# Kernel tuning notes

Measured on AMD Instinct MI355X. Metric: run time of the kernel, lower is better.

The kernel has to match this reference:

```python
import jax, jax.numpy as jnp
import numpy as np

B, SORB, H, L = 32768, 64, 256, 2


def setup_inputs() -> dict:
    key = jax.random.key(0)
    ks = jax.random.split(key, 11)
    s = 1.0 / np.sqrt(H)

    def u(k, shape):
        return jax.random.uniform(k, shape, jnp.float32, -s, s)

    return {
        "x": jax.random.randint(ks[0], (B, SORB), 0, 2).astype(jnp.int32),
        # PyTorch GRU params, gate order (r, z, n); layer 0 input_size=2, layer 1 input_size=H
        "w_ih0": u(ks[1], (3 * H, 2)), "w_hh0": u(ks[2], (3 * H, H)),
        "b_ih0": u(ks[3], (3 * H,)), "b_hh0": u(ks[4], (3 * H,)),
        "w_ih1": u(ks[5], (3 * H, H)), "w_hh1": u(ks[6], (3 * H, H)),
        "b_ih1": u(ks[7], (3 * H,)), "b_hh1": u(ks[8], (3 * H,)),
        "w_amp": u(ks[9], (2, H)), "b_amp": u(ks[10], (2,)),
    }


def _gru_cell(x, h, w_ih, w_hh, b_ih, b_hh):
    # PyTorch GRUCell math, gates in (r, z, n) order
    gi = x @ w_ih.T + b_ih
    gh = h @ w_hh.T + b_hh
    ir, iz, i_n = jnp.split(gi, 3, axis=-1)
    hr, hz, h_n = jnp.split(gh, 3, axis=-1)
    r = jax.nn.sigmoid(ir + hr)
    z = jax.nn.sigmoid(iz + hz)
    n = jnp.tanh(i_n + r * h_n)
    return (1.0 - z) * n + z * h


def reference(x, w_ih0, w_hh0, b_ih0, b_hh0, w_ih1, w_hh1, b_ih1, b_hh1, w_amp, b_amp):
    bits = x  # [B, SORB], values in {0,1} (equals ((+-1)+1)/2 of original input)
    nb = bits.shape[0]
    layer_params = [(w_ih0, w_hh0, b_ih0, b_hh0), (w_ih1, w_hh1, b_ih1, b_hh1)]

    def stacked(inp, h):  # h: [L, B, H]
        hs = []
        for l, (wi, wh, bi, bh) in enumerate(layer_params):
            hl = _gru_cell(inp, h[l], wi, wh, bi, bh)
            hs.append(hl)
            inp = hl
        return inp, jnp.stack(hs)

    h0 = jnp.zeros((L, nb, H), jnp.float32)
    # priming step with zero input (x0 = zeros(nbatch,1,2))
    _, h = stacked(jnp.zeros((nb, 2), jnp.float32), h0)

    def step(h, b_t):  # b_t: [B]
        onehot = jax.nn.one_hot(b_t, 2, dtype=jnp.float32)
        y, h = stacked(onehot, h)
        amp = jax.nn.softmax(y @ w_amp.T + b_amp, axis=1)  # [B, 2]
        p = jnp.sum(amp * onehot, axis=1)  # conditional prob of the sampled bit
        return h, p

    _, probs = jax.lax.scan(step, h, bits.T)  # probs: [SORB, B]
    return jnp.sqrt(jnp.prod(probs, axis=0))  # wavefunction amplitude, [B]
```

## Files before the change

kernel.cpp:

```cpp
#include <hip/hip_runtime.h>

typedef _Float16 f16;
typedef _Float16 f16x8 __attribute__((ext_vector_type(8)));
typedef float f32x4 __attribute__((ext_vector_type(4)));

#define H_    256
#define TB_   64
#define NT_   1024
#define SORB_ 64
#define SLOT_ 8192

#define MFMA16(a, b, c) __builtin_amdgcn_mfma_f32_16x16x32_f16((a), (b), (c), 0, 0, 0)
#define UNR _Pragma("unroll")

__device__ __forceinline__ float sigm(float v) {
  return __builtin_amdgcn_rcpf(1.0f + __builtin_amdgcn_exp2f(v * -1.442695040888963f));
}
__device__ __forceinline__ float tanh_fast(float v) {
  float a = fabsf(v);
  float e = __builtin_amdgcn_exp2f(a * -2.885390081777927f);
  float t = (1.0f - e) * __builtin_amdgcn_rcpf(1.0f + e);
  return copysignf(t, v);
}
__device__ __forceinline__ int lswz(int lrow, int col) {
  return lrow * H_ + (col ^ ((lrow & 7) << 3));
}

__global__ void wcvt(const float* __restrict__ a, const float* __restrict__ b,
                     const float* __restrict__ c, f16* __restrict__ o) {
  int i = blockIdx.x * 256 + threadIdx.x;
  const int n = 768 * 256;
  if (i < n) {
    o[i]         = (f16)a[i];
    o[n + i]     = (f16)b[i];
    o[2 * n + i] = (f16)c[i];
  }
}

__global__ __launch_bounds__(NT_, 4) void rnnwf(
    const int* __restrict__ x,
    const float* __restrict__ w_ih0, const float* __restrict__ b_ih0,
    const float* __restrict__ b_hh0, const float* __restrict__ b_ih1,
    const float* __restrict__ b_hh1, const float* __restrict__ w_amp,
    const float* __restrict__ b_amp, const f16* __restrict__ W16,
    float* __restrict__ out)
{
  __shared__ __align__(16) f16 hall[6 * SLOT_];
  __shared__ float wampL[512];
  __shared__ unsigned short bitsL[TB_ * 4];
  __shared__ unsigned long long bitsT[SORB_];

  const int tid  = threadIdx.x;
  const int wave = tid >> 6;
  const int lane = tid & 63;
  const int l15  = lane & 15;
  const int lg   = lane >> 4;
  const int lg4  = lg << 2;
  const int col  = wave * 16 + l15;
  const int rowbase = blockIdx.x * TB_;

  for (int j = tid; j < 512; j += NT_) wampL[j] = w_amp[j];
  if (tid < 256) {
    int row = tid >> 2, q = tid & 3;
    const int* xp = x + (size_t)(rowbase + row) * SORB_ + q * 16;
    unsigned m = 0;
    #pragma unroll
    for (int i = 0; i < 16; ++i) m |= (unsigned)(xp[i] & 1) << i;
    bitsL[row * 4 + q] = (unsigned short)m;
  }
  for (int i = tid; i < 6 * SLOT_; i += NT_) hall[i] = (f16)0.f;

  const float baseR = b_ih0[col]       + b_hh0[col];
  const float baseZ = b_ih0[256 + col] + b_hh0[256 + col];
  const float baseN = b_ih0[512 + col];
  const float wR0 = w_ih0[2 * col + 0],         wR1 = w_ih0[2 * col + 1];
  const float wZ0 = w_ih0[2 * (256 + col) + 0], wZ1 = w_ih0[2 * (256 + col) + 1];
  const float wN0 = w_ih0[2 * (512 + col) + 0], wN1 = w_ih0[2 * (512 + col) + 1];
  const float sumR0 = baseR + wR0, dR = wR1 - wR0;
  const float sumZ0 = baseZ + wZ0, dZ = wZ1 - wZ0;
  const float sumN0 = baseN + wN0, dN = wN1 - wN0;
  const float bhh0n_c = b_hh0[512 + col];
  const float b1r_c   = b_ih1[col]       + b_hh1[col];
  const float b1z_c   = b_ih1[256 + col] + b_hh1[256 + col];
  const float b1ni_c  = b_ih1[512 + col];
  const float b1nh_c  = b_hh1[512 + col];
  const float ba0 = b_amp[0], ba1 = b_amp[1];
  __syncthreads();

  if (tid < SORB_) {
    unsigned long long mk = 0ull;
    const int q = tid >> 4, sh = tid & 15;
    #pragma unroll 4
    for (int r = 0; r < TB_; ++r)
      mk |= (unsigned long long)((bitsL[r * 4 + q] >> sh) & 1) << r;
    bitsT[tid] = mk;
  }
  __syncthreads();

  float prob = 1.0f;
  const f16* Wih1 = W16 + 768 * 256;
  const f16* Whh1 = W16 + 2 * 768 * 256;
  const f16* p0base = W16  + col * 256;
  const f16* pibase = Wih1 + col * 256;
  const f16* phbase = Whh1 + col * 256;

  const int hrow = tid >> 4;
  const int t16  = tid & 15;
  const int hsh  = hrow & 31;
  const bool hhi = hrow >= 32;

  int pa = 0, pb = 2 * SLOT_, pc = 4 * SLOT_;

  for (int t = -1; t < SORB_; ++t) {
    unsigned lo32 = 0u, hi32 = 0u;
    if (t >= 0) {
      unsigned long long mk = bitsT[t];
      lo32 = (unsigned)mk; hi32 = (unsigned)(mk >> 32);
    }

    {
      f32x4 aR[4], aZ[4], aN[4];
      UNR for (int m = 0; m < 4; ++m) { aR[m] = (f32x4){0,0,0,0}; aZ[m] = aR[m]; aN[m] = aR[m]; }
      #pragma unroll 2
      for (int kt = 0; kt < 8; ++kt) {
        const int k0 = kt * 32 + lg * 8;
        f16x8 Br = *(const f16x8*)(p0base + k0);
        f16x8 Bz = *(const f16x8*)(p0base + 65536 + k0);
        f16x8 Bn = *(const f16x8*)(p0base + 131072 + k0);
        UNR for (int m = 0; m < 4; ++m) {
          f16x8 A = *(const f16x8*)&hall[pa + (m >> 1) * SLOT_ + lswz((m & 1) * 16 + l15, k0)];
          aR[m] = MFMA16(A, Br, aR[m]);
          aZ[m] = MFMA16(A, Bz, aZ[m]);
          aN[m] = MFMA16(A, Bn, aN[m]);
        }
      }
      if (t >= 0) {
        UNR for (int m = 0; m < 4; ++m) {
          const unsigned hsel = (m < 2) ? lo32 : hi32;
          UNR for (int e = 0; e < 4; ++e) {
            const int lrow = (m & 1) * 16 + lg4 + e;
            float fb = (float)((hsel >> ((m & 1) * 16 + lg4 + e)) & 1u);
            float giR = fmaf(fb, dR, sumR0);
            float giZ = fmaf(fb, dZ, sumZ0);
            float giN = fmaf(fb, dN, sumN0);
            float r  = sigm(aR[m][e] + giR);
            float z  = sigm(aZ[m][e] + giZ);
            float n  = tanh_fast(giN + r * (aN[m][e] + bhh0n_c));
            float ho = (float)hall[pa + (m >> 1) * SLOT_ + lswz(lrow, col)];
            hall[pc + (m >> 1) * SLOT_ + lswz(lrow, col)] = (f16)((1.0f - z) * n + z * ho);
          }
        }
      } else {
        UNR for (int m = 0; m < 4; ++m) {
          UNR for (int e = 0; e < 4; ++e) {
            const int lrow = (m & 1) * 16 + lg4 + e;
            float r  = sigm(aR[m][e] + baseR);
            float z  = sigm(aZ[m][e] + baseZ);
            float n  = tanh_fast(baseN + r * (aN[m][e] + bhh0n_c));
            float ho = (float)hall[pa + (m >> 1) * SLOT_ + lswz(lrow, col)];
            hall[pc + (m >> 1) * SLOT_ + lswz(lrow, col)] = (f16)((1.0f - z) * n + z * ho);
          }
        }
      }
    }
    __syncthreads();

    {
      f32x4 tR[4], tZ[4], tNi[4], tNh[4];
      UNR for (int m = 0; m < 4; ++m) {
        tR[m] = (f32x4){0,0,0,0}; tZ[m] = tR[m]; tNi[m] = tR[m]; tNh[m] = tR[m];
      }
      #pragma unroll 1
      for (int kt = 0; kt < 8; ++kt) {
        const int k0 = kt * 32 + lg * 8;
        {
          f16x8 BiR = *(const f16x8*)(pibase + k0);
          f16x8 BiZ = *(const f16x8*)(pibase + 65536 + k0);
          f16x8 BiN = *(const f16x8*)(pibase + 131072 + k0);
          UNR for (int m = 0; m < 4; ++m) {
            f16x8 A0 = *(const f16x8*)&hall[pc + (m >> 1) * SLOT_ + lswz((m & 1) * 16 + l15, k0)];
            tR[m]  = MFMA16(A0, BiR, tR[m]);
            tZ[m]  = MFMA16(A0, BiZ, tZ[m]);
            tNi[m] = MFMA16(A0, BiN, tNi[m]);
          }
        }
        {
          f16x8 BhR = *(const f16x8*)(phbase + k0);
          f16x8 BhZ = *(const f16x8*)(phbase + 65536 + k0);
          f16x8 BhN = *(const f16x8*)(phbase + 131072 + k0);
          UNR for (int m = 0; m < 4; ++m) {
            f16x8 A1 = *(const f16x8*)&hall[pb + (m >> 1) * SLOT_ + lswz((m & 1) * 16 + l15, k0)];
            tR[m]  = MFMA16(A1, BhR, tR[m]);
            tZ[m]  = MFMA16(A1, BhZ, tZ[m]);
            tNh[m] = MFMA16(A1, BhN, tNh[m]);
          }
        }
      }
      UNR for (int m = 0; m < 4; ++m) {
        UNR for (int e = 0; e < 4; ++e) {
          const int lrow = (m & 1) * 16 + lg4 + e;
          float r  = sigm(tR[m][e] + b1r_c);
          float z  = sigm(tZ[m][e] + b1z_c);
          float n  = tanh_fast(tNi[m][e] + b1ni_c + r * (tNh[m][e] + b1nh_c));
          float ho = (float)hall[pb + (m >> 1) * SLOT_ + lswz(lrow, col)];
          hall[pa + (m >> 1) * SLOT_ + lswz(lrow, col)] = (f16)((1.0f - z) * n + z * ho);
        }
      }
    }
    __syncthreads();

    if (t >= 0) {
      float d0 = 0.f, d1 = 0.f;
      #pragma unroll
      for (int j = 0; j < 2; ++j) {
        const int k0 = t16 * 16 + j * 8;
        f16x8 hv = *(const f16x8*)&hall[pa + (hrow >> 5) * SLOT_ + lswz(hrow & 31, k0)];
        f32x4 w0a = *(const f32x4*)&wampL[k0];
        f32x4 w0b = *(const f32x4*)&wampL[k0 + 4];
        f32x4 w1a = *(const f32x4*)&wampL[256 + k0];
        f32x4 w1b = *(const f32x4*)&wampL[256 + k0 + 4];
        #pragma unroll
        for (int i = 0; i < 4; ++i) {
          float hfa = (float)hv[i], hfb = (float)hv[4 + i];
          d0 = fmaf(hfa, w0a[i], d0); d0 = fmaf(hfb, w0b[i], d0);
          d1 = fmaf(hfa, w1a[i], d1); d1 = fmaf(hfb, w1b[i], d1);
        }
      }
      d0 += __shfl_xor(d0, 1); d0 += __shfl_xor(d0, 2);
      d0 += __shfl_xor(d0, 4); d0 += __shfl_xor(d0, 8);
      d1 += __shfl_xor(d1, 1); d1 += __shfl_xor(d1, 2);
      d1 += __shfl_xor(d1, 4); d1 += __shfl_xor(d1, 8);
      const unsigned hm = hhi ? hi32 : lo32;
      const int bit = (hm >> hsh) & 1;
      float diff = (d0 + ba0) - (d1 + ba1);
      if (bit) diff = -diff;
      prob *= __builtin_amdgcn_rcpf(1.0f + __builtin_amdgcn_exp2f(diff * -1.442695040888963f));
    }

    int tmp = pa; pa = pc; pc = pb; pb = tmp;
  }

  if (t16 == 0) out[rowbase + hrow] = sqrtf(prob);
}

extern "C" void kernel_launch(void* const* d_in, const int* in_sizes, int n_in,
                              void* d_out, int out_size, void* d_ws, size_t ws_size,
                              hipStream_t stream) {
  const int*   x     = (const int*)d_in[0];
  const float* w_ih0 = (const float*)d_in[1];
  const float* w_hh0 = (const float*)d_in[2];
  const float* b_ih0 = (const float*)d_in[3];
  const float* b_hh0 = (const float*)d_in[4];
  const float* w_ih1 = (const float*)d_in[5];
  const float* w_hh1 = (const float*)d_in[6];
  const float* b_ih1 = (const float*)d_in[7];
  const float* b_hh1 = (const float*)d_in[8];
  const float* w_amp = (const float*)d_in[9];
  const float* b_amp = (const float*)d_in[10];
  (void)in_sizes; (void)n_in; (void)out_size; (void)ws_size;

  f16* W16 = (f16*)d_ws;
  hipLaunchKernelGGL(wcvt, dim3(768), dim3(256), 0, stream, w_hh0, w_ih1, w_hh1, W16);
  hipLaunchKernelGGL(rnnwf, dim3(32768 / TB_), dim3(NT_), 0, stream,
                     x, w_ih0, b_ih0, b_hh0, b_ih1, b_hh1, w_amp, b_amp, W16,
                     (float*)d_out);
}
```

Before: 4.961 ms.

## Halve block threads, stage hidden states in registers to cut LDS footprint

Reduces the block from 1024 to 512 threads, so each wave now computes two 16-column tiles. The rotating three-buffer hidden-state scheme (six slots) becomes a fixed two-buffer scheme (four slots): new layer outputs are held in registers, then written back after a barrier. Per-column biases and input weights move into an LDS table instead of per-thread registers. The smaller LDS footprint is meant to let more blocks co-reside per CU so one block's barriers overlap another's compute. The cost is two extra barriers per timestep and higher register pressure from the staged outputs.

```diff
diff --git a/kernel.cpp b/kernel.cpp
--- a/kernel.cpp
+++ b/kernel.cpp
@@ -2,11 +2,12 @@
 
 typedef _Float16 f16;
 typedef _Float16 f16x8 __attribute__((ext_vector_type(8)));
+typedef _Float16 f16x4 __attribute__((ext_vector_type(4)));
 typedef float f32x4 __attribute__((ext_vector_type(4)));
 
 #define H_    256
 #define TB_   64
-#define NT_   1024
+#define NT_   512
 #define SORB_ 64
 #define SLOT_ 8192
 
@@ -45,9 +46,9 @@
     const float* __restrict__ b_amp, const f16* __restrict__ W16,
     float* __restrict__ out)
 {
-  __shared__ __align__(16) f16 hall[6 * SLOT_];
+  __shared__ __align__(16) f16 hall[4 * SLOT_];
+  __shared__ float tabL[11 * 256];
   __shared__ float wampL[512];
-  __shared__ unsigned short bitsL[TB_ * 4];
   __shared__ unsigned long long bitsT[SORB_];
 
   const int tid  = threadIdx.x;
@@ -60,56 +61,50 @@
   const int rowbase = blockIdx.x * TB_;
 
   for (int j = tid; j < 512; j += NT_) wampL[j] = w_amp[j];
-  if (tid < 256) {
-    int row = tid >> 2, q = tid & 3;
-    const int* xp = x + (size_t)(rowbase + row) * SORB_ + q * 16;
+  for (int j = tid; j < 256; j += NT_) {
+    float bR = b_ih0[j] + b_hh0[j];
+    float bZ = b_ih0[256 + j] + b_hh0[256 + j];
+    float bN = b_ih0[512 + j];
+    float r0 = w_ih0[2 * j],           r1 = w_ih0[2 * j + 1];
+    float z0 = w_ih0[2 * (256 + j)],   z1 = w_ih0[2 * (256 + j) + 1];
+    float n0 = w_ih0[2 * (512 + j)],   n1 = w_ih0[2 * (512 + j) + 1];
+    tabL[j]          = bR + r0;  tabL[256 + j]  = r1 - r0;
+    tabL[512 + j]    = bZ + z0;  tabL[768 + j]  = z1 - z0;
+    tabL[1024 + j]   = bN + n0;  tabL[1280 + j] = n1 - n0;
+    tabL[1536 + j]   = b_hh0[512 + j];
+    tabL[1792 + j]   = b_ih1[j] + b_hh1[j];
+    tabL[2048 + j]   = b_ih1[256 + j] + b_hh1[256 + j];
+    tabL[2304 + j]   = b_ih1[512 + j];
+    tabL[2560 + j]   = b_hh1[512 + j];
+  }
+  if (tid < TB_ * 4) {
+    const int* xp = x + (size_t)(rowbase + (tid >> 2)) * SORB_ + (tid & 3) * 16;
     unsigned m = 0;
     #pragma unroll
     for (int i = 0; i < 16; ++i) m |= (unsigned)(xp[i] & 1) << i;
-    bitsL[row * 4 + q] = (unsigned short)m;
-  }
-  for (int i = tid; i < 6 * SLOT_; i += NT_) hall[i] = (f16)0.f;
-
-  const float baseR = b_ih0[col]       + b_hh0[col];
-  const float baseZ = b_ih0[256 + col] + b_hh0[256 + col];
-  const float baseN = b_ih0[512 + col];
-  const float wR0 = w_ih0[2 * col + 0],         wR1 = w_ih0[2 * col + 1];
-  const float wZ0 = w_ih0[2 * (256 + col) + 0], wZ1 = w_ih0[2 * (256 + col) + 1];
-  const float wN0 = w_ih0[2 * (512 + col) + 0], wN1 = w_ih0[2 * (512 + col) + 1];
-  const float sumR0 = baseR + wR0, dR = wR1 - wR0;
-  const float sumZ0 = baseZ + wZ0, dZ = wZ1 - wZ0;
-  const float sumN0 = baseN + wN0, dN = wN1 - wN0;
-  const float bhh0n_c = b_hh0[512 + col];
-  const float b1r_c   = b_ih1[col]       + b_hh1[col];
-  const float b1z_c   = b_ih1[256 + col] + b_hh1[256 + col];
-  const float b1ni_c  = b_ih1[512 + col];
-  const float b1nh_c  = b_hh1[512 + col];
-  const float ba0 = b_amp[0], ba1 = b_amp[1];
+    ((unsigned short*)hall)[tid] = (unsigned short)m;
+  }
   __syncthreads();
-
   if (tid < SORB_) {
     unsigned long long mk = 0ull;
     const int q = tid >> 4, sh = tid & 15;
     #pragma unroll 4
     for (int r = 0; r < TB_; ++r)
-      mk |= (unsigned long long)((bitsL[r * 4 + q] >> sh) & 1) << r;
+      mk |= (unsigned long long)((((const unsigned short*)hall)[r * 4 + q] >> sh) & 1) << r;
     bitsT[tid] = mk;
   }
+  const unsigned long long hmk = ((const unsigned long long*)hall)[tid >> 3];
   __syncthreads();
+  for (int i = tid; i < 4 * SLOT_; i += NT_) hall[i] = (f16)0.f;
+  const float ba0 = b_amp[0], ba1 = b_amp[1];
+  __syncthreads();
 
   float prob = 1.0f;
-  const f16* Wih1 = W16 + 768 * 256;
-  const f16* Whh1 = W16 + 2 * 768 * 256;
-  const f16* p0base = W16  + col * 256;
-  const f16* pibase = Wih1 + col * 256;
-  const f16* phbase = Whh1 + col * 256;
-
-  const int hrow = tid >> 4;
-  const int t16  = tid & 15;
-  const int hsh  = hrow & 31;
-  const bool hhi = hrow >= 32;
-
-  int pa = 0, pb = 2 * SLOT_, pc = 4 * SLOT_;
+  const f16* p0base = W16 + col * 256;
+  const f16* pibase = W16 + 768 * 256 + col * 256;
+  const f16* phbase = W16 + 2 * 768 * 256 + col * 256;
+  const int hrow = tid >> 3;
+  const int t8   = tid & 7;
 
   for (int t = -1; t < SORB_; ++t) {
     unsigned lo32 = 0u, hi32 = 0u;
@@ -118,54 +113,73 @@
       lo32 = (unsigned)mk; hi32 = (unsigned)(mk >> 32);
     }
 
-    {
+    f16x4 s0[8];
+    UNR for (int nt = 0; nt < 2; ++nt) {
+      const int c = col + nt * 128;
+      const f16* pw = p0base + nt * 32768;
       f32x4 aR[4], aZ[4], aN[4];
       UNR for (int m = 0; m < 4; ++m) { aR[m] = (f32x4){0,0,0,0}; aZ[m] = aR[m]; aN[m] = aR[m]; }
       #pragma unroll 2
       for (int kt = 0; kt < 8; ++kt) {
         const int k0 = kt * 32 + lg * 8;
-        f16x8 Br = *(const f16x8*)(p0base + k0);
-        f16x8 Bz = *(const f16x8*)(p0base + 65536 + k0);
-        f16x8 Bn = *(const f16x8*)(p0base + 131072 + k0);
+        f16x8 Br = *(const f16x8*)(pw + k0);
+        f16x8 Bz = *(const f16x8*)(pw + 65536 + k0);
+        f16x8 Bn = *(const f16x8*)(pw + 131072 + k0);
         UNR for (int m = 0; m < 4; ++m) {
-          f16x8 A = *(const f16x8*)&hall[pa + (m >> 1) * SLOT_ + lswz((m & 1) * 16 + l15, k0)];
+          f16x8 A = *(const f16x8*)&hall[(m >> 1) * SLOT_ + lswz((m & 1) * 16 + l15, k0)];
           aR[m] = MFMA16(A, Br, aR[m]);
           aZ[m] = MFMA16(A, Bz, aZ[m]);
           aN[m] = MFMA16(A, Bn, aN[m]);
         }
       }
       if (t >= 0) {
+        const float sR = tabL[c],        dRv = tabL[256 + c];
+        const float sZ = tabL[512 + c],  dZv = tabL[768 + c];
+        const float sN = tabL[1024 + c], dNv = tabL[1280 + c];
+        const float bh0n = tabL[1536 + c];
         UNR for (int m = 0; m < 4; ++m) {
           const unsigned hsel = (m < 2) ? lo32 : hi32;
           UNR for (int e = 0; e < 4; ++e) {
             const int lrow = (m & 1) * 16 + lg4 + e;
             float fb = (float)((hsel >> ((m & 1) * 16 + lg4 + e)) & 1u);
-            float giR = fmaf(fb, dR, sumR0);
-            float giZ = fmaf(fb, dZ, sumZ0);
-            float giN = fmaf(fb, dN, sumN0);
-            float r  = sigm(aR[m][e] + giR);
-            float z  = sigm(aZ[m][e] + giZ);
-            float n  = tanh_fast(giN + r * (aN[m][e] + bhh0n_c));
-            float ho = (float)hall[pa + (m >> 1) * SLOT_ + lswz(lrow, col)];
-            hall[pc + (m >> 1) * SLOT_ + lswz(lrow, col)] = (f16)((1.0f - z) * n + z * ho);
+            float r  = sigm(aR[m][e] + fmaf(fb, dRv, sR));
+            float z  = sigm(aZ[m][e] + fmaf(fb, dZv, sZ));
+            float n  = tanh_fast(fmaf(fb, dNv, sN) + r * (aN[m][e] + bh0n));
+            float ho = (float)hall[(m >> 1) * SLOT_ + lswz(lrow, c)];
+            s0[nt * 4 + m][e] = (f16)((1.0f - z) * n + z * ho);
           }
         }
       } else {
+        const float pR = b_ih0[c] + b_hh0[c];
+        const float pZ = b_ih0[256 + c] + b_hh0[256 + c];
+        const float pN = b_ih0[512 + c];
+        const float bh0n = b_hh0[512 + c];
         UNR for (int m = 0; m < 4; ++m) {
           UNR for (int e = 0; e < 4; ++e) {
             const int lrow = (m & 1) * 16 + lg4 + e;
-            float r  = sigm(aR[m][e] + baseR);
-            float z  = sigm(aZ[m][e] + baseZ);
-            float n  = tanh_fast(baseN + r * (aN[m][e] + bhh0n_c));
-            float ho = (float)hall[pa + (m >> 1) * SLOT_ + lswz(lrow, col)];
-            hall[pc + (m >> 1) * SLOT_ + lswz(lrow, col)] = (f16)((1.0f - z) * n + z * ho);
-          }
-        }
-      }
-    }
-    __syncthreads();
-
-    {
+            float r  = sigm(aR[m][e] + pR);
+            float z  = sigm(aZ[m][e] + pZ);
+            float n  = tanh_fast(pN + r * (aN[m][e] + bh0n));
+            float ho = (float)hall[(m >> 1) * SLOT_ + lswz(lrow, c)];
+            s0[nt * 4 + m][e] = (f16)((1.0f - z) * n + z * ho);
+          }
+        }
+      }
+    }
+    __syncthreads();
+    UNR for (int nt = 0; nt < 2; ++nt) {
+      const int c = col + nt * 128;
+      UNR for (int m = 0; m < 4; ++m)
+        UNR for (int e = 0; e < 4; ++e)
+          hall[(m >> 1) * SLOT_ + lswz((m & 1) * 16 + lg4 + e, c)] = s0[nt * 4 + m][e];
+    }
+    __syncthreads();
+
+    f16x4 s1[8];
+    UNR for (int nt = 0; nt < 2; ++nt) {
+      const int c = col + nt * 128;
+      const f16* pib = pibase + nt * 32768;
+      const f16* phb = phbase + nt * 32768;
       f32x4 tR[4], tZ[4], tNi[4], tNh[4];
       UNR for (int m = 0; m < 4; ++m) {
         tR[m] = (f32x4){0,0,0,0}; tZ[m] = tR[m]; tNi[m] = tR[m]; tNh[m] = tR[m];
@@ -174,47 +188,56 @@
       for (int kt = 0; kt < 8; ++kt) {
         const int k0 = kt * 32 + lg * 8;
         {
-          f16x8 BiR = *(const f16x8*)(pibase + k0);
-          f16x8 BiZ = *(const f16x8*)(pibase + 65536 + k0);
-          f16x8 BiN = *(const f16x8*)(pibase + 131072 + k0);
+          f16x8 BiR = *(const f16x8*)(pib + k0);
+          f16x8 BiZ = *(const f16x8*)(pib + 65536 + k0);
+          f16x8 BiN = *(const f16x8*)(pib + 131072 + k0);
           UNR for (int m = 0; m < 4; ++m) {
-            f16x8 A0 = *(const f16x8*)&hall[pc + (m >> 1) * SLOT_ + lswz((m & 1) * 16 + l15, k0)];
+            f16x8 A0 = *(const f16x8*)&hall[(m >> 1) * SLOT_ + lswz((m & 1) * 16 + l15, k0)];
             tR[m]  = MFMA16(A0, BiR, tR[m]);
             tZ[m]  = MFMA16(A0, BiZ, tZ[m]);
             tNi[m] = MFMA16(A0, BiN, tNi[m]);
           }
         }
         {
-          f16x8 BhR = *(const f16x8*)(phbase + k0);
-          f16x8 BhZ = *(const f16x8*)(phbase + 65536 + k0);
-          f16x8 BhN = *(const f16x8*)(phbase + 131072 + k0);
+          f16x8 BhR = *(const f16x8*)(phb + k0);
+          f16x8 BhZ = *(const f16x8*)(phb + 65536 + k0);
+          f16x8 BhN = *(const f16x8*)(phb + 131072 + k0);
           UNR for (int m = 0; m < 4; ++m) {
-            f16x8 A1 = *(const f16x8*)&hall[pb + (m >> 1) * SLOT_ + lswz((m & 1) * 16 + l15, k0)];
+            f16x8 A1 = *(const f16x8*)&hall[2 * SLOT_ + (m >> 1) * SLOT_ + lswz((m & 1) * 16 + l15, k0)];
             tR[m]  = MFMA16(A1, BhR, tR[m]);
             tZ[m]  = MFMA16(A1, BhZ, tZ[m]);
             tNh[m] = MFMA16(A1, BhN, tNh[m]);
           }
         }
       }
+      const float c1r  = tabL[1792 + c], c1z  = tabL[2048 + c];
+      const float c1ni = tabL[2304 + c], c1nh = tabL[2560 + c];
       UNR for (int m = 0; m < 4; ++m) {
         UNR for (int e = 0; e < 4; ++e) {
           const int lrow = (m & 1) * 16 + lg4 + e;
-          float r  = sigm(tR[m][e] + b1r_c);
-          float z  = sigm(tZ[m][e] + b1z_c);
-          float n  = tanh_fast(tNi[m][e] + b1ni_c + r * (tNh[m][e] + b1nh_c));
-          float ho = (float)hall[pb + (m >> 1) * SLOT_ + lswz(lrow, col)];
-          hall[pa + (m >> 1) * SLOT_ + lswz(lrow, col)] = (f16)((1.0f - z) * n + z * ho);
-        }
-      }
+          float r  = sigm(tR[m][e] + c1r);
+          float z  = sigm(tZ[m][e] + c1z);
+          float n  = tanh_fast(tNi[m][e] + c1ni + r * (tNh[m][e] + c1nh));
+          float ho = (float)hall[2 * SLOT_ + (m >> 1) * SLOT_ + lswz(lrow, c)];
+          s1[nt * 4 + m][e] = (f16)((1.0f - z) * n + z * ho);
+        }
+      }
+    }
+    __syncthreads();
+    UNR for (int nt = 0; nt < 2; ++nt) {
+      const int c = col + nt * 128;
+      UNR for (int m = 0; m < 4; ++m)
+        UNR for (int e = 0; e < 4; ++e)
+          hall[2 * SLOT_ + (m >> 1) * SLOT_ + lswz((m & 1) * 16 + lg4 + e, c)] = s1[nt * 4 + m][e];
     }
     __syncthreads();
 
     if (t >= 0) {
       float d0 = 0.f, d1 = 0.f;
       #pragma unroll
-      for (int j = 0; j < 2; ++j) {
-        const int k0 = t16 * 16 + j * 8;
-        f16x8 hv = *(const f16x8*)&hall[pa + (hrow >> 5) * SLOT_ + lswz(hrow & 31, k0)];
+      for (int j = 0; j < 4; ++j) {
+        const int k0 = t8 * 32 + j * 8;
+        f16x8 hv = *(const f16x8*)&hall[2 * SLOT_ + (hrow >> 5) * SLOT_ + lswz(hrow & 31, k0)];
         f32x4 w0a = *(const f32x4*)&wampL[k0];
         f32x4 w0b = *(const f32x4*)&wampL[k0 + 4];
         f32x4 w1a = *(const f32x4*)&wampL[256 + k0];
@@ -226,21 +249,16 @@
           d1 = fmaf(hfa, w1a[i], d1); d1 = fmaf(hfb, w1b[i], d1);
         }
       }
-      d0 += __shfl_xor(d0, 1); d0 += __shfl_xor(d0, 2);
-      d0 += __shfl_xor(d0, 4); d0 += __shfl_xor(d0, 8);
-      d1 += __shfl_xor(d1, 1); d1 += __shfl_xor(d1, 2);
-      d1 += __shfl_xor(d1, 4); d1 += __shfl_xor(d1, 8);
-      const unsigned hm = hhi ? hi32 : lo32;
-      const int bit = (hm >> hsh) & 1;
+      d0 += __shfl_xor(d0, 1); d0 += __shfl_xor(d0, 2); d0 += __shfl_xor(d0, 4);
+      d1 += __shfl_xor(d1, 1); d1 += __shfl_xor(d1, 2); d1 += __shfl_xor(d1, 4);
+      const int bit = (unsigned)(hmk >> t) & 1u;
       float diff = (d0 + ba0) - (d1 + ba1);
       if (bit) diff = -diff;
       prob *= __builtin_amdgcn_rcpf(1.0f + __builtin_amdgcn_exp2f(diff * -1.442695040888963f));
     }
-
-    int tmp = pa; pa = pc; pc = pb; pb = tmp;
-  }
-
-  if (t16 == 0) out[rowbase + hrow] = sqrtf(prob);
+  }
+
+  if (t8 == 0) out[rowbase + hrow] = sqrtf(prob);
 }
 
 extern "C" void kernel_launch(void* const* d_in, const int* in_sizes, int n_in,
```

Result: slower. 7.092 ms (+43.0%).
